# Kernel optimization log

Hardware: AMD Instinct MI355X
Metric: run time of the kernel (lower is better)

The kernel has to match this reference:

```python
import jax, jax.numpy as jnp
import numpy as np

CUTOFF = 5.0
BOX = 20.0
EPS = 1e-5


def _neighbor_list_np(cutoff, coords, cell):
    # coords: [N,3] float32, cell: [3,3]. Returns (pair_first, pair_second, pair_image)
    inv_cell = np.linalg.inv(cell)
    proj = coords @ inv_cell
    frac = np.fmod(proj, 1.0)                      # matches torch.fmod (sign-preserving)
    woff = np.floor(proj).astype(np.int64)          # torch.div(..., rounding_mode='floor')
    wrapped = (frac @ cell).astype(coords.dtype)
    inv_lengths = np.linalg.norm(inv_cell, axis=0)
    nb = (np.floor(cutoff * inv_lengths + EPS) + 1).astype(np.int64)
    ranges = [np.arange(-int(n), int(n) + 1) for n in nb]
    # image grid ordered (i1 outer, i2, i3 inner) to match the nested torch loops
    images = np.stack(np.meshgrid(*ranges, indexing='ij'), axis=-1).reshape(-1, 3)
    off_cart = images.astype(coords.dtype) @ cell   # [K,3]
    drij = wrapped[:, None, :] - wrapped[None, :, :]           # [N,N,3]
    diff = drij[None, :, :, :] + off_cart[:, None, None, :]    # [K,N,N,3]
    dist = np.linalg.norm(diff, axis=-1)                       # [K,N,N]
    mask = dist < cutoff
    zero_k = int(np.where((images == 0).all(axis=1))[0][0])
    np.fill_diagonal(mask[zero_k], False)                      # drop self pairs in home image
    k, i, j = np.nonzero(mask)  # row-major (k,i,j) == per-image blocks of (i,j), same order as torch
    woff_ij = woff[i] - woff[j]
    pair_image = images[k] - woff_ij
    return i, j, pair_image


def setup_inputs() -> dict:
    key = jax.random.key(0)
    n_mol, n_at = 16, 512
    coordinates = jax.random.uniform(key, (n_mol, n_at, 3), dtype=jnp.float32) * BOX
    nonblank = jnp.ones((n_mol, n_at), dtype=bool)
    real_atoms = jnp.arange(n_mol * n_at, dtype=jnp.int32)
    inv_real_atoms = jnp.arange(n_mol * n_at, dtype=jnp.int32)
    cell = jnp.tile((BOX * jnp.eye(3, dtype=jnp.float32))[None], (n_mol, 1, 1))
    mol_index = jnp.arange(n_mol * n_at, dtype=jnp.int32) // n_at
    return dict(coordinates=coordinates, nonblank=nonblank, real_atoms=real_atoms,
                inv_real_atoms=inv_real_atoms, cell=cell, mol_index=mol_index,
                n_molecules=n_mol, n_atoms_max=n_at)


def reference(coordinates, nonblank, real_atoms, inv_real_atoms, cell, mol_index,
              n_molecules, n_atoms_max):
    # --- neighbor-list construction (torch.no_grad section): host numpy, vectorized over images ---
    coords_np = np.asarray(coordinates)
    cell_np = np.asarray(cell)
    nb_np = np.asarray(nonblank)
    pfs, pss, ofs = [], [], []
    for m in range(n_molecules):
        r = coords_np[m][nb_np[m]]
        pf, ps, of = _neighbor_list_np(CUTOFF, r, cell_np[m])
        if len(pf) == 0:
            continue
        pfs.append(pf + m * n_atoms_max)
        pss.append(ps + m * n_atoms_max)
        ofs.append(of)
    pf = np.concatenate(pfs)
    ps = np.concatenate(pss)
    of = np.concatenate(ofs)
    n_images = max(1, int(np.abs(of).max()))

    pair_first = inv_real_atoms[jnp.asarray(pf)]
    pair_second = inv_real_atoms[jnp.asarray(ps)]
    offsets = jnp.asarray(of.astype(np.int32))
    n_off = 2 * n_images + 1
    o1, o2, o3 = (offsets + n_images).T
    offset_index = o3 + n_off * (o2 + n_off * o1)
    pair_mol = mol_index[pair_first]
    pair_cell = cell[pair_mol]                                   # [P,3,3]
    pair_offsets = jnp.einsum('pk,pkl->pl', offsets.astype(cell.dtype), pair_cell)

    # --- differentiable distance evaluation ---
    coordflat = coordinates.reshape(n_molecules * n_atoms_max, 3)[real_atoms]
    paircoord = coordflat[pair_first] - coordflat[pair_second] + pair_offsets
    distflat2 = jnp.linalg.norm(paircoord, axis=1)
    return distflat2, pair_first, pair_second, paircoord, offsets, offset_index
```

## Files before the change

kernel.cpp:

```cpp
#include <hip/hip_runtime.h>

#define NMOL 16
#define NAT  512
#define NK   27

#define SSMAX 24.999998092651367f

__device__ __forceinline__ float wrap1(float v) {
    return __fmul_rn(__fmul_rn(v, 0.05f), 20.0f);
}

__device__ __forceinline__ bool probe(float dx, float dy, float dz,
                                      int& ox, int& oy, int& oz,
                                      float& cx, float& cy, float& cz) {
    ox = (dx > 15.0f) ? -1 : ((dx < -15.0f) ? 1 : 0);
    oy = (dy > 15.0f) ? -1 : ((dy < -15.0f) ? 1 : 0);
    oz = (dz > 15.0f) ? -1 : ((dz < -15.0f) ? 1 : 0);
    cx = 20.0f * (float)ox;
    cy = 20.0f * (float)oy;
    cz = 20.0f * (float)oz;
    float ax = __fadd_rn(dx, cx);
    float ay = __fadd_rn(dy, cy);
    float az = __fadd_rn(dz, cz);
    float ss = __fadd_rn(__fadd_rn(__fmul_rn(ax, ax), __fmul_rn(ay, ay)),
                         __fmul_rn(az, az));
    return ss < SSMAX;
}

__global__ __launch_bounds__(256, 8) void pass_count(const float* __restrict__ coords,
                                                     int* __restrict__ cnt) {
    __shared__ float w4[NAT * 4];
    __shared__ int   cur[4][NK];
    const int blk = blockIdx.x;
    const int m   = blk >> 7;
    const int ig  = blk & 127;
    const int t   = threadIdx.x;
    const int w   = t >> 6;
    const int lane = t & 63;
    const int i   = ig * 4 + w;

    const float* cm = coords + (size_t)m * NAT * 3;
    for (int q = t; q < NAT * 3; q += 256) {
        int a = q / 3, c = q - a * 3;
        w4[a * 4 + c] = wrap1(cm[q]);
    }
    if (t < 4 * NK) cur[t / NK][t % NK] = 0;
    __syncthreads();

    const float wx = w4[i * 4 + 0];
    const float wy = w4[i * 4 + 1];
    const float wz = w4[i * 4 + 2];
    const float4* w4p = reinterpret_cast<const float4*>(w4);

    #pragma unroll
    for (int it = 0; it < NAT / 64; ++it) {
        const int j = it * 64 + lane;
        float4 wj = w4p[j];
        float dx = __fsub_rn(wx, wj.x);
        float dy = __fsub_rn(wy, wj.y);
        float dz = __fsub_rn(wz, wj.z);
        int ox, oy, oz; float cx, cy, cz;
        bool hit = probe(dx, dy, dz, ox, oy, oz, cx, cy, cz) && (j != i);
        if (hit) {
            int k = (ox + 1) * 9 + (oy + 1) * 3 + (oz + 1);
            atomicAdd(&cur[w][k], 1);
        }
    }
    __syncthreads();

    if (t < 4 * NK) {
        int ww = t / NK, k = t % NK;
        cnt[(m * NK + k) * NAT + (ig * 4 + ww)] = cur[ww][k];
    }
}

__global__ __launch_bounds__(512) void scan_chunk(int* __restrict__ cnt,
                                                  int* __restrict__ sums) {
    __shared__ int buf[512];
    const int c = blockIdx.x;
    const int t = threadIdx.x;
    const int idx = c * 512 + t;
    buf[t] = cnt[idx];
    __syncthreads();
    for (int d = 1; d < 512; d <<= 1) {
        int v = (t >= d) ? buf[t - d] : 0;
        __syncthreads();
        buf[t] += v;
        __syncthreads();
    }
    cnt[idx] = (t == 0) ? 0 : buf[t - 1];
    if (t == 511) sums[c] = buf[511];
}

__global__ __launch_bounds__(256, 8) void pass_emit(const float* __restrict__ coords,
                                                    const int* __restrict__ cnt,
                                                    const int* __restrict__ sums,
                                                    float* __restrict__ out, int P) {
    __shared__ float w4[NAT * 4];
    __shared__ float r4[NAT * 4];
    __shared__ int   sbuf[512];
    __shared__ int   cur[4][NK];
    const int blk = blockIdx.x;
    const int m   = blk >> 7;
    const int ig  = blk & 127;
    const int t   = threadIdx.x;
    const int w   = t >> 6;
    const int lane = t & 63;
    const int i   = ig * 4 + w;

    const float* cm = coords + (size_t)m * NAT * 3;
    for (int q = t; q < NAT * 3; q += 256) {
        int a = q / 3, c = q - a * 3;
        float v = cm[q];
        r4[a * 4 + c] = v;
        w4[a * 4 + c] = wrap1(v);
    }
    {
        int v0 = (t < NMOL * NK) ? sums[t] : 0;
        int t2 = t + 256;
        int v1 = (t2 < NMOL * NK) ? sums[t2] : 0;
        sbuf[t] = v0;
        sbuf[t2] = v1;
    }
    __syncthreads();
    for (int d = 1; d < 512; d <<= 1) {
        int a0 = (t >= d) ? sbuf[t - d] : 0;
        int t2 = t + 256;
        int a1 = sbuf[t2 - d];
        __syncthreads();
        sbuf[t]  += a0;
        sbuf[t2] += a1;
        __syncthreads();
    }
    if (t < 4 * NK) {
        int ww = t / NK, k = t % NK;
        int c  = m * NK + k;
        int gbase = (c == 0) ? 0 : sbuf[c - 1];
        cur[ww][k] = cnt[c * NAT + (ig * 4 + ww)] + gbase;
    }
    __syncthreads();

    const float wx = w4[i * 4 + 0];
    const float wy = w4[i * 4 + 1];
    const float wz = w4[i * 4 + 2];
    const float rx = r4[i * 4 + 0];
    const float ry = r4[i * 4 + 1];
    const float rz = r4[i * 4 + 2];
    const float4* w4p = reinterpret_cast<const float4*>(w4);
    const float4* r4p = reinterpret_cast<const float4*>(r4);
    const int pf = m * NAT + i;
    const unsigned long long ltmask =
        (lane == 0) ? 0ull : (~0ull >> (64 - lane));

    for (int it = 0; it < NAT / 64; ++it) {
        const int j = it * 64 + lane;
        float4 wj = w4p[j];
        float dx = __fsub_rn(wx, wj.x);
        float dy = __fsub_rn(wy, wj.y);
        float dz = __fsub_rn(wz, wj.z);
        int ox, oy, oz; float cx, cy, cz;
        bool hit = probe(dx, dy, dz, ox, oy, oz, cx, cy, cz) && (j != i);
        int kk = hit ? ((ox + 1) * 9 + (oy + 1) * 3 + (oz + 1)) : 0;

        unsigned long long grp = __ballot(hit);
        #pragma unroll
        for (int b = 0; b < 5; ++b) {
            unsigned long long bm = __ballot((kk >> b) & 1);
            grp &= ((kk >> b) & 1) ? bm : ~bm;
        }
        int leader = hit ? (__ffsll((unsigned long long)grp) - 1) : 0;
        int cntg   = __popcll(grp);
        int rank   = __popcll(grp & ltmask);

        int base = 0;
        if (hit && lane == leader)
            base = atomicAdd(&cur[w][kk], cntg);
        base = __shfl(base, leader, 64);

        if (hit) {
            int p = base + rank;
            if (p < P) {
                float4 rj = r4p[j];
                float px = __fadd_rn(__fsub_rn(rx, rj.x), cx);
                float py = __fadd_rn(__fsub_rn(ry, rj.y), cy);
                float pz = __fadd_rn(__fsub_rn(rz, rj.z), cz);
                float ss = __fadd_rn(__fadd_rn(__fmul_rn(px, px), __fmul_rn(py, py)),
                                     __fmul_rn(pz, pz));
                out[p]                 = __fsqrt_rn(ss);
                out[P + p]             = (float)pf;
                out[2 * P + p]         = (float)(m * NAT + j);
                out[3 * P + 3 * p + 0] = px;
                out[3 * P + 3 * p + 1] = py;
                out[3 * P + 3 * p + 2] = pz;
                out[6 * P + 3 * p + 0] = (float)ox;
                out[6 * P + 3 * p + 1] = (float)oy;
                out[6 * P + 3 * p + 2] = (float)oz;
                out[9 * P + p]         = (float)kk;
            }
        }
    }
}

extern "C" void kernel_launch(void* const* d_in, const int* in_sizes, int n_in,
                              void* d_out, int out_size, void* d_ws, size_t ws_size,
                              hipStream_t stream) {
    const float* coords = (const float*)d_in[0];
    int* cnt  = (int*)d_ws;
    int* sums = cnt + NMOL * NK * NAT;
    float* out = (float*)d_out;
    const int P = out_size / 10;

    hipLaunchKernelGGL(pass_count, dim3(NMOL * NAT / 4), dim3(256), 0, stream, coords, cnt);
    hipLaunchKernelGGL(scan_chunk, dim3(NMOL * NK), dim3(512), 0, stream, cnt, sums);
    hipLaunchKernelGGL(pass_emit, dim3(NMOL * NAT / 4), dim3(256), 0, stream,
                       coords, cnt, sums, out, P);
}
```

Baseline: 96.36 us.

## Fuse count, scan and emit into one persistent kernel with grid barriers

Merges the three kernels into a single kernel of 1024 blocks that synchronise through atomic grid barriers. Each block now handles two atom groups, and the per-pair image codes from the count phase stay in registers so the emit phase does not recompute the distance probes. This removes two kernel launches and the repeated probe arithmetic. In exchange it adds a memset, spin-wait barriers that deadlock unless all blocks are co-resident, and lower occupancy from launch_bounds(256,4).

```diff
diff --git a/kernel.cpp b/kernel.cpp
--- a/kernel.cpp
+++ b/kernel.cpp
@@ -3,6 +3,8 @@
 #define NMOL 16
 #define NAT  512
 #define NK   27
+#define NCHUNK (NMOL * NK)
+#define NBLK 1024
 
 #define SSMAX 24.999998092651367f
 
@@ -10,192 +12,192 @@
     return __fmul_rn(__fmul_rn(v, 0.05f), 20.0f);
 }
 
-__device__ __forceinline__ bool probe(float dx, float dy, float dz,
-                                      int& ox, int& oy, int& oz,
-                                      float& cx, float& cy, float& cz) {
-    ox = (dx > 15.0f) ? -1 : ((dx < -15.0f) ? 1 : 0);
-    oy = (dy > 15.0f) ? -1 : ((dy < -15.0f) ? 1 : 0);
-    oz = (dz > 15.0f) ? -1 : ((dz < -15.0f) ? 1 : 0);
-    cx = 20.0f * (float)ox;
-    cy = 20.0f * (float)oy;
-    cz = 20.0f * (float)oz;
-    float ax = __fadd_rn(dx, cx);
-    float ay = __fadd_rn(dy, cy);
-    float az = __fadd_rn(dz, cz);
+__device__ __forceinline__ int probe_code(float wx, float wy, float wz,
+                                          float4 wj, bool self) {
+    float dx = __fsub_rn(wx, wj.x);
+    float dy = __fsub_rn(wy, wj.y);
+    float dz = __fsub_rn(wz, wj.z);
+    int ox = (dx > 15.0f) ? -1 : ((dx < -15.0f) ? 1 : 0);
+    int oy = (dy > 15.0f) ? -1 : ((dy < -15.0f) ? 1 : 0);
+    int oz = (dz > 15.0f) ? -1 : ((dz < -15.0f) ? 1 : 0);
+    float ax = __fadd_rn(dx, 20.0f * (float)ox);
+    float ay = __fadd_rn(dy, 20.0f * (float)oy);
+    float az = __fadd_rn(dz, 20.0f * (float)oz);
     float ss = __fadd_rn(__fadd_rn(__fmul_rn(ax, ax), __fmul_rn(ay, ay)),
                          __fmul_rn(az, az));
-    return ss < SSMAX;
-}
-
-__global__ __launch_bounds__(256, 8) void pass_count(const float* __restrict__ coords,
-                                                     int* __restrict__ cnt) {
-    __shared__ float w4[NAT * 4];
-    __shared__ int   cur[4][NK];
-    const int blk = blockIdx.x;
-    const int m   = blk >> 7;
-    const int ig  = blk & 127;
-    const int t   = threadIdx.x;
-    const int w   = t >> 6;
+    bool hit = (ss < SSMAX) && !self;
+    int kk = (ox + 1) * 9 + (oy + 1) * 3 + (oz + 1);
+    return hit ? kk : 31;
+}
+
+__device__ __forceinline__ void grid_barrier(int* ctr, int target) {
+    __syncthreads();
+    if (threadIdx.x == 0) {
+        __hip_atomic_fetch_add(ctr, 1, __ATOMIC_ACQ_REL, __HIP_MEMORY_SCOPE_AGENT);
+        while (__hip_atomic_load(ctr, __ATOMIC_ACQUIRE, __HIP_MEMORY_SCOPE_AGENT) < target)
+            __builtin_amdgcn_s_sleep(8);
+    }
+    __syncthreads();
+}
+
+__global__ __launch_bounds__(256, 4) void fused(const float* __restrict__ coords,
+                                                int* __restrict__ cnt,
+                                                int* __restrict__ sums,
+                                                int* __restrict__ bar,
+                                                float* __restrict__ out, int P) {
+    __shared__ float r4[NAT * 4];
+    __shared__ union { float w4[NAT * 4]; int sbuf[512]; } u;
+    __shared__ int cur[2][4][NK];
+
+    const int blk  = blockIdx.x;
+    const int m    = blk >> 6;
+    const int g0   = (blk & 63) * 2;
+    const int t    = threadIdx.x;
+    const int w    = t >> 6;
     const int lane = t & 63;
-    const int i   = ig * 4 + w;
-
-    const float* cm = coords + (size_t)m * NAT * 3;
-    for (int q = t; q < NAT * 3; q += 256) {
-        int a = q / 3, c = q - a * 3;
-        w4[a * 4 + c] = wrap1(cm[q]);
-    }
-    if (t < 4 * NK) cur[t / NK][t % NK] = 0;
-    __syncthreads();
-
-    const float wx = w4[i * 4 + 0];
-    const float wy = w4[i * 4 + 1];
-    const float wz = w4[i * 4 + 2];
-    const float4* w4p = reinterpret_cast<const float4*>(w4);
-
-    #pragma unroll
-    for (int it = 0; it < NAT / 64; ++it) {
-        const int j = it * 64 + lane;
-        float4 wj = w4p[j];
-        float dx = __fsub_rn(wx, wj.x);
-        float dy = __fsub_rn(wy, wj.y);
-        float dz = __fsub_rn(wz, wj.z);
-        int ox, oy, oz; float cx, cy, cz;
-        bool hit = probe(dx, dy, dz, ox, oy, oz, cx, cy, cz) && (j != i);
-        if (hit) {
-            int k = (ox + 1) * 9 + (oy + 1) * 3 + (oz + 1);
-            atomicAdd(&cur[w][k], 1);
-        }
-    }
-    __syncthreads();
-
-    if (t < 4 * NK) {
-        int ww = t / NK, k = t % NK;
-        cnt[(m * NK + k) * NAT + (ig * 4 + ww)] = cur[ww][k];
-    }
-}
-
-__global__ __launch_bounds__(512) void scan_chunk(int* __restrict__ cnt,
-                                                  int* __restrict__ sums) {
-    __shared__ int buf[512];
-    const int c = blockIdx.x;
-    const int t = threadIdx.x;
-    const int idx = c * 512 + t;
-    buf[t] = cnt[idx];
-    __syncthreads();
-    for (int d = 1; d < 512; d <<= 1) {
-        int v = (t >= d) ? buf[t - d] : 0;
-        __syncthreads();
-        buf[t] += v;
-        __syncthreads();
-    }
-    cnt[idx] = (t == 0) ? 0 : buf[t - 1];
-    if (t == 511) sums[c] = buf[511];
-}
-
-__global__ __launch_bounds__(256, 8) void pass_emit(const float* __restrict__ coords,
-                                                    const int* __restrict__ cnt,
-                                                    const int* __restrict__ sums,
-                                                    float* __restrict__ out, int P) {
-    __shared__ float w4[NAT * 4];
-    __shared__ float r4[NAT * 4];
-    __shared__ int   sbuf[512];
-    __shared__ int   cur[4][NK];
-    const int blk = blockIdx.x;
-    const int m   = blk >> 7;
-    const int ig  = blk & 127;
-    const int t   = threadIdx.x;
-    const int w   = t >> 6;
-    const int lane = t & 63;
-    const int i   = ig * 4 + w;
+    const int iA   = g0 * 4 + w;
+    const int iB   = iA + 4;
 
     const float* cm = coords + (size_t)m * NAT * 3;
     for (int q = t; q < NAT * 3; q += 256) {
         int a = q / 3, c = q - a * 3;
         float v = cm[q];
         r4[a * 4 + c] = v;
-        w4[a * 4 + c] = wrap1(v);
-    }
-    {
-        int v0 = (t < NMOL * NK) ? sums[t] : 0;
-        int t2 = t + 256;
-        int v1 = (t2 < NMOL * NK) ? sums[t2] : 0;
-        sbuf[t] = v0;
-        sbuf[t2] = v1;
-    }
-    __syncthreads();
-    for (int d = 1; d < 512; d <<= 1) {
-        int a0 = (t >= d) ? sbuf[t - d] : 0;
-        int t2 = t + 256;
-        int a1 = sbuf[t2 - d];
-        __syncthreads();
-        sbuf[t]  += a0;
-        sbuf[t2] += a1;
-        __syncthreads();
-    }
-    if (t < 4 * NK) {
-        int ww = t / NK, k = t % NK;
-        int c  = m * NK + k;
-        int gbase = (c == 0) ? 0 : sbuf[c - 1];
-        cur[ww][k] = cnt[c * NAT + (ig * 4 + ww)] + gbase;
-    }
-    __syncthreads();
-
-    const float wx = w4[i * 4 + 0];
-    const float wy = w4[i * 4 + 1];
-    const float wz = w4[i * 4 + 2];
-    const float rx = r4[i * 4 + 0];
-    const float ry = r4[i * 4 + 1];
-    const float rz = r4[i * 4 + 2];
-    const float4* w4p = reinterpret_cast<const float4*>(w4);
-    const float4* r4p = reinterpret_cast<const float4*>(r4);
-    const int pf = m * NAT + i;
-    const unsigned long long ltmask =
-        (lane == 0) ? 0ull : (~0ull >> (64 - lane));
-
+        u.w4[a * 4 + c] = wrap1(v);
+    }
+    if (t < 2 * 4 * NK) ((int*)cur)[t] = 0;
+    __syncthreads();
+
+    const float wxA = u.w4[iA * 4 + 0], wyA = u.w4[iA * 4 + 1], wzA = u.w4[iA * 4 + 2];
+    const float wxB = u.w4[iB * 4 + 0], wyB = u.w4[iB * 4 + 1], wzB = u.w4[iB * 4 + 2];
+    const float4* w4p = reinterpret_cast<const float4*>(u.w4);
+
+    unsigned long long codeA = 0, codeB = 0;
+    #pragma unroll
     for (int it = 0; it < NAT / 64; ++it) {
         const int j = it * 64 + lane;
         float4 wj = w4p[j];
-        float dx = __fsub_rn(wx, wj.x);
-        float dy = __fsub_rn(wy, wj.y);
-        float dz = __fsub_rn(wz, wj.z);
-        int ox, oy, oz; float cx, cy, cz;
-        bool hit = probe(dx, dy, dz, ox, oy, oz, cx, cy, cz) && (j != i);
-        int kk = hit ? ((ox + 1) * 9 + (oy + 1) * 3 + (oz + 1)) : 0;
-
-        unsigned long long grp = __ballot(hit);
+        int cA = probe_code(wxA, wyA, wzA, wj, j == iA);
+        int cB = probe_code(wxB, wyB, wzB, wj, j == iB);
+        codeA |= (unsigned long long)cA << (8 * it);
+        codeB |= (unsigned long long)cB << (8 * it);
+        if (cA != 31) atomicAdd(&cur[0][w][cA], 1);
+        if (cB != 31) atomicAdd(&cur[1][w][cB], 1);
+    }
+    __syncthreads();
+    if (t < 216) {
+        int uu = t / 108, rem = t % 108, ww = rem / 27, k = rem % 27;
+        int i = (g0 + uu) * 4 + ww;
+        cnt[(m * NK + k) * NAT + i] = cur[uu][ww][k];
+    }
+    grid_barrier(bar, NBLK);
+
+    if (blk < NCHUNK) {
+        int* sb = u.sbuf;
+        const int i0 = blk * 512 + t;
+        sb[t]       = cnt[i0];
+        sb[t + 256] = cnt[i0 + 256];
+        __syncthreads();
+        for (int d = 1; d < 512; d <<= 1) {
+            int a0 = (t >= d) ? sb[t - d] : 0;
+            int a1 = sb[t + 256 - d];
+            __syncthreads();
+            sb[t] += a0;
+            sb[t + 256] += a1;
+            __syncthreads();
+        }
+        cnt[i0]       = (t == 0) ? 0 : sb[t - 1];
+        cnt[i0 + 256] = sb[t + 255];
+        if (t == 255) sums[blk] = sb[511];
+    }
+    grid_barrier(bar, 2 * NBLK);
+
+    {
+        int v0 = sums[t];
+        int t2 = t + 256;
+        int v1 = (t2 < NCHUNK) ? sums[t2] : 0;
+        u.sbuf[t]  = v0;
+        u.sbuf[t2] = v1;
+    }
+    __syncthreads();
+    for (int d = 1; d < 512; d <<= 1) {
+        int a0 = (t >= d) ? u.sbuf[t - d] : 0;
+        int a1 = u.sbuf[t + 256 - d];
+        __syncthreads();
+        u.sbuf[t] += a0;
+        u.sbuf[t + 256] += a1;
+        __syncthreads();
+    }
+    if (t < 216) {
+        int uu = t / 108, rem = t % 108, ww = rem / 27, k = rem % 27;
+        int c  = m * NK + k;
+        int gbase = (c == 0) ? 0 : u.sbuf[c - 1];
+        int i = (g0 + uu) * 4 + ww;
+        cur[uu][ww][k] = cnt[c * NAT + i] + gbase;
+    }
+    __syncthreads();
+
+    const float4* r4p = reinterpret_cast<const float4*>(r4);
+    const unsigned long long ltmask =
+        (lane == 0) ? 0ull : (~0ull >> (64 - lane));
+
+    #pragma unroll
+    for (int uu = 0; uu < 2; ++uu) {
+        const int i  = (g0 + uu) * 4 + w;
+        const float rx = r4[i * 4 + 0], ry = r4[i * 4 + 1], rz = r4[i * 4 + 2];
+        const int pf = m * NAT + i;
+        const unsigned long long code8 = (uu == 0) ? codeA : codeB;
+
         #pragma unroll
-        for (int b = 0; b < 5; ++b) {
-            unsigned long long bm = __ballot((kk >> b) & 1);
-            grp &= ((kk >> b) & 1) ? bm : ~bm;
-        }
-        int leader = hit ? (__ffsll((unsigned long long)grp) - 1) : 0;
-        int cntg   = __popcll(grp);
-        int rank   = __popcll(grp & ltmask);
-
-        int base = 0;
-        if (hit && lane == leader)
-            base = atomicAdd(&cur[w][kk], cntg);
-        base = __shfl(base, leader, 64);
-
-        if (hit) {
-            int p = base + rank;
-            if (p < P) {
-                float4 rj = r4p[j];
-                float px = __fadd_rn(__fsub_rn(rx, rj.x), cx);
-                float py = __fadd_rn(__fsub_rn(ry, rj.y), cy);
-                float pz = __fadd_rn(__fsub_rn(rz, rj.z), cz);
-                float ss = __fadd_rn(__fadd_rn(__fmul_rn(px, px), __fmul_rn(py, py)),
-                                     __fmul_rn(pz, pz));
-                out[p]                 = __fsqrt_rn(ss);
-                out[P + p]             = (float)pf;
-                out[2 * P + p]         = (float)(m * NAT + j);
-                out[3 * P + 3 * p + 0] = px;
-                out[3 * P + 3 * p + 1] = py;
-                out[3 * P + 3 * p + 2] = pz;
-                out[6 * P + 3 * p + 0] = (float)ox;
-                out[6 * P + 3 * p + 1] = (float)oy;
-                out[6 * P + 3 * p + 2] = (float)oz;
-                out[9 * P + p]         = (float)kk;
+        for (int it = 0; it < NAT / 64; ++it) {
+            const int j = it * 64 + lane;
+            int code = (int)((code8 >> (8 * it)) & 0xffull);
+            bool hit = (code != 31);
+            int kk = hit ? code : 0;
+
+            unsigned long long grp = __ballot(hit);
+            #pragma unroll
+            for (int b = 0; b < 5; ++b) {
+                unsigned long long bm = __ballot((kk >> b) & 1);
+                grp &= ((kk >> b) & 1) ? bm : ~bm;
+            }
+            int leader = hit ? (__ffsll((unsigned long long)grp) - 1) : 0;
+            int cntg   = __popcll(grp);
+            int rank   = __popcll(grp & ltmask);
+
+            int base = 0;
+            if (hit && lane == leader)
+                base = atomicAdd(&cur[uu][w][kk], cntg);
+            base = __shfl(base, leader, 64);
+
+            if (hit) {
+                int p = base + rank;
+                if (p < P) {
+                    int ox = kk / 9;
+                    int rem = kk - ox * 9;
+                    int oy = rem / 3;
+                    int oz = rem - oy * 3;
+                    ox -= 1; oy -= 1; oz -= 1;
+                    float cx = 20.0f * (float)ox;
+                    float cy = 20.0f * (float)oy;
+                    float cz = 20.0f * (float)oz;
+                    float4 rj = r4p[j];
+                    float px = __fadd_rn(__fsub_rn(rx, rj.x), cx);
+                    float py = __fadd_rn(__fsub_rn(ry, rj.y), cy);
+                    float pz = __fadd_rn(__fsub_rn(rz, rj.z), cz);
+                    float ss = __fadd_rn(__fadd_rn(__fmul_rn(px, px), __fmul_rn(py, py)),
+                                         __fmul_rn(pz, pz));
+                    out[p]                 = __fsqrt_rn(ss);
+                    out[P + p]             = (float)pf;
+                    out[2 * P + p]         = (float)(m * NAT + j);
+                    out[3 * P + 3 * p + 0] = px;
+                    out[3 * P + 3 * p + 1] = py;
+                    out[3 * P + 3 * p + 2] = pz;
+                    out[6 * P + 3 * p + 0] = (float)ox;
+                    out[6 * P + 3 * p + 1] = (float)oy;
+                    out[6 * P + 3 * p + 2] = (float)oz;
+                    out[9 * P + p]         = (float)kk;
+                }
             }
         }
     }
@@ -204,14 +206,15 @@
 extern "C" void kernel_launch(void* const* d_in, const int* in_sizes, int n_in,
                               void* d_out, int out_size, void* d_ws, size_t ws_size,
                               hipStream_t stream) {
+    (void)in_sizes; (void)n_in; (void)ws_size;
     const float* coords = (const float*)d_in[0];
     int* cnt  = (int*)d_ws;
     int* sums = cnt + NMOL * NK * NAT;
+    int* bar  = sums + 448;
     float* out = (float*)d_out;
-    const int P = out_size / 10;
-
-    hipLaunchKernelGGL(pass_count, dim3(NMOL * NAT / 4), dim3(256), 0, stream, coords, cnt);
-    hipLaunchKernelGGL(scan_chunk, dim3(NMOL * NK), dim3(512), 0, stream, cnt, sums);
-    hipLaunchKernelGGL(pass_emit, dim3(NMOL * NAT / 4), dim3(256), 0, stream,
-                       coords, cnt, sums, out, P);
-}
+    int P = out_size / 10;
+
+    hipMemsetAsync(bar, 0, 64, stream);
+    hipLaunchKernelGGL(fused, dim3(NBLK), dim3(256), 0, stream,
+                       coords, cnt, sums, bar, out, P);
+}
```

Measured after the change: 219.6 us. +127.9%, slower.
